# Kernel tuning notes

Measured on AMD Instinct MI355X. Metric: run time of the kernel, lower is better.

## Reference

```python
import jax, jax.numpy as jnp
import numpy as np

B, L, C, H = 2, 4096, 1024, 16
D = C // H
KERNEL_FROM_KN = lambda kn: int(np.sqrt(kn)) + 1


def setup_inputs() -> dict:
    key = jax.random.key(0)
    ks = jax.random.split(key, 4)
    s = 0.02
    kk = KERNEL_FROM_KN(144)  # 13
    return {
        "x": jax.random.normal(ks[0], (B, L, C), jnp.float32),
        "w_qkv": jax.random.normal(ks[1], (C, 3 * C), jnp.float32) * s,
        "b_qkv": jnp.zeros((3 * C,), jnp.float32),
        "rpb": jax.random.normal(ks[2], (H, 2 * kk - 1), jnp.float32) * s,
        "w_proj": jax.random.normal(ks[3], (C, C), jnp.float32) * s,
        "b_proj": jnp.zeros((C,), jnp.float32),
        "k_neighbors": 144,
    }


def reference(x, w_qkv, b_qkv, rpb, w_proj, b_proj, k_neighbors):
    kk = KERNEL_FROM_KN(k_neighbors)  # kernel size (13)
    scale = D ** -0.5
    qkv = (x @ w_qkv + b_qkv).reshape(B, L, 3, H, D).transpose(2, 0, 3, 1, 4)  # (3,B,H,L,D)
    q, k, v = qkv[0] * scale, qkv[1], qkv[2]
    pos = jnp.arange(L)
    # NATTEN window: centered, clamped so the full kernel fits inside [0, L)
    start = jnp.clip(pos - kk // 2, 0, L - kk)               # (L,)
    idx = start[:, None] + jnp.arange(kk)[None, :]           # (L,kk) key positions
    k_win = k[:, :, idx, :]                                  # (B,H,L,kk,D)
    v_win = v[:, :, idx, :]                                  # (B,H,L,kk,D)
    attn = jnp.einsum('bhld,bhlkd->bhlk', q, k_win)          # (B,H,L,kk)
    # relative-position bias index = key_pos - query_pos + (kk - 1) in [0, 2kk-2]
    bias_idx = idx - pos[:, None] + (kk - 1)                 # (L,kk)
    attn = attn + rpb[:, bias_idx][None]                     # broadcast over batch
    attn = jax.nn.softmax(attn, axis=-1)
    out = jnp.einsum('bhlk,bhlkd->bhld', attn, v_win)        # (B,H,L,D)
    out = out.transpose(0, 2, 1, 3).reshape(B, L, C)
    return out @ w_proj + b_proj
```

## Files before the change

### kernel.cpp

```cpp
#include <hip/hip_runtime.h>
#include <hip/hip_bf16.h>
#include <stdint.h>

typedef __bf16 bf16x8 __attribute__((ext_vector_type(8)));
typedef float floatx4 __attribute__((ext_vector_type(4)));

#define B_ 2
#define L_ 4096
#define C_ 1024
#define H_ 16
#define D_ 64
constexpr size_t TEN = (size_t)B_ * H_ * L_ * D_;

__device__ __forceinline__ float bf2f(unsigned short u) {
  union { unsigned int i; float f; } x; x.i = ((unsigned int)u) << 16; return x.f;
}
__device__ __forceinline__ unsigned short f2bf(float f) {
  union { float f; unsigned int i; } x; x.f = f;
  unsigned int i = x.i;
  return (unsigned short)((i + 0x7FFFu + ((i >> 16) & 1u)) >> 16);
}

__device__ __forceinline__ void async_copy16(const unsigned short* g, unsigned short* l) {
  __builtin_amdgcn_global_load_lds(
      (const __attribute__((address_space(1))) unsigned int*)g,
      (__attribute__((address_space(3))) unsigned int*)l,
      16, 0, 0);
}

__global__ __launch_bounds__(256) void cvt_f32_bf16_kernel(
    const float* __restrict__ in, unsigned short* __restrict__ out, int n) {
  int i = (blockIdx.x * 256 + threadIdx.x) * 8;
  if (i >= n) return;
  float4 a = *(const float4*)&in[i];
  float4 b = *(const float4*)&in[i + 4];
  union { uint4 u; unsigned short s[8]; } st;
  st.s[0] = f2bf(a.x); st.s[1] = f2bf(a.y); st.s[2] = f2bf(a.z); st.s[3] = f2bf(a.w);
  st.s[4] = f2bf(b.x); st.s[5] = f2bf(b.y); st.s[6] = f2bf(b.z); st.s[7] = f2bf(b.w);
  *(uint4*)&out[i] = st.u;
}

__global__ __launch_bounds__(256) void transpose_f32_bf16(
    const float* __restrict__ in, unsigned short* __restrict__ out,
    int R, int Ccols) {
  __shared__ float tile[64][65];
  const int bx = blockIdx.x * 64;
  const int by = blockIdx.y * 64;
  const int t = threadIdx.x;
  for (int i = t; i < 1024; i += 256) {
    int r = i >> 4, c4 = (i & 15) << 2;
    float4 v = *(const float4*)&in[(size_t)(by + r) * Ccols + bx + c4];
    tile[r][c4] = v.x; tile[r][c4 + 1] = v.y; tile[r][c4 + 2] = v.z; tile[r][c4 + 3] = v.w;
  }
  __syncthreads();
  for (int i = t; i < 512; i += 256) {
    int r = i >> 3, c8 = (i & 7) << 3;
    union { uint4 u; unsigned short s[8]; } st;
    #pragma unroll
    for (int j = 0; j < 8; ++j) st.s[j] = f2bf(tile[c8 + j][r]);
    *(uint4*)&out[(size_t)(bx + r) * R + by + c8] = st.u;
  }
}

template <int MODE>
__global__ __launch_bounds__(512, 2) void gemm256_kernel(
    const unsigned short* __restrict__ A, const unsigned short* __restrict__ Bt,
    const float* __restrict__ bias, unsigned short* __restrict__ out_bf,
    float* __restrict__ out_f, int M, int N, int K, float qscale) {
  constexpr int BK = 64;
  __shared__ unsigned short ash0[256 * BK], ash1[256 * BK], ash2[256 * BK];
  __shared__ unsigned short bsh0[128 * BK], bsh1[128 * BK], bsh2[128 * BK];

  const int t = threadIdx.x;
  const int nwgx = gridDim.x;
  const int nwg = nwgx * gridDim.y;
  const int flat = blockIdx.y * nwgx + blockIdx.x;
  const int cpx = nwg >> 3;
  const int swz = (flat & 7) * cpx + (flat >> 3);
  const int n0 = (swz % nwgx) * 128;
  const int m0 = (swz / nwgx) * 256;

  const int wave = t >> 6, lane = t & 63;
  const int wr = wave >> 1;
  const int wc = wave & 1;
  const int lm = lane & 15, quad = lane >> 4;

  floatx4 acc[4][4];
  #pragma unroll
  for (int i = 0; i < 4; ++i)
    #pragma unroll
    for (int j = 0; j < 4; ++j) acc[i][j] = (floatx4)0.0f;

#define STAGE(KT, SA, SB) do { \
    _Pragma("unroll") \
    for (int q = 0; q < 4; ++q) { \
      int off = (q * 512 + t) * 8; \
      int r_ = off >> 6; \
      int c_ = (off & 63) ^ ((r_ & 7) << 3); \
      async_copy16(&A[(size_t)(m0 + r_) * K + (KT) + c_], &SA[off]); \
    } \
    _Pragma("unroll") \
    for (int q = 0; q < 2; ++q) { \
      int off = (q * 512 + t) * 8; \
      int r_ = off >> 6; \
      int c_ = (off & 63) ^ ((r_ & 7) << 3); \
      async_copy16(&Bt[(size_t)(n0 + r_) * K + (KT) + c_], &SB[off]); \
    } \
  } while (0)

#define PHASE(ASH, BSH, NH, TAILSTMT) do { \
    bf16x8 af[4][2], bfr[2][2]; \
    _Pragma("unroll") \
    for (int i = 0; i < 4; ++i) { \
      int ra = wr * 64 + i * 16 + lm; \
      _Pragma("unroll") \
      for (int k = 0; k < 2; ++k) \
        af[i][k] = *(const bf16x8*)&ASH[ra * 64 + ((k * 32 + quad * 8) ^ ((ra & 7) << 3))]; \
    } \
    _Pragma("unroll") \
    for (int j = 0; j < 2; ++j) { \
      int rb = wc * 64 + (NH) * 32 + j * 16 + lm; \
      _Pragma("unroll") \
      for (int k = 0; k < 2; ++k) \
        bfr[j][k] = *(const bf16x8*)&BSH[rb * 64 + ((k * 32 + quad * 8) ^ ((rb & 7) << 3))]; \
    } \
    asm volatile("" ::: "memory"); \
    __builtin_amdgcn_s_barrier(); \
    __builtin_amdgcn_s_setprio(1); \
    _Pragma("unroll") \
    for (int k = 0; k < 2; ++k) \
      _Pragma("unroll") \
      for (int i = 0; i < 4; ++i) \
        _Pragma("unroll") \
        for (int j = 0; j < 2; ++j) \
          acc[i][(NH) * 2 + j] = \
              __builtin_amdgcn_mfma_f32_16x16x32_bf16(af[i][k], bfr[j][k], acc[i][(NH) * 2 + j], 0, 0, 0); \
    __builtin_amdgcn_s_setprio(0); \
    TAILSTMT \
    asm volatile("" ::: "memory"); \
    __builtin_amdgcn_s_barrier(); \
  } while (0)

#define WAIT6 asm volatile("s_waitcnt vmcnt(6)" ::: "memory");
#define WAIT0 asm volatile("s_waitcnt vmcnt(0)" ::: "memory");

#define TILE(KT2, ASH, BSH, SAN, SBN, DO_STAGE, TAILSTMT) do { \
    if (DO_STAGE) STAGE((KT2), SAN, SBN); \
    PHASE(ASH, BSH, 0, ;); \
    PHASE(ASH, BSH, 1, TAILSTMT); \
  } while (0)

  STAGE(0, ash0, bsh0);
  STAGE(BK, ash1, bsh1);
  WAIT6
  asm volatile("" ::: "memory");
  __builtin_amdgcn_s_barrier();

  for (int g = 0; g < 4; ++g) {
    int kb = g * 3 * BK;
    TILE(kb + 2 * BK, ash0, bsh0, ash2, bsh2, true, WAIT6);
    TILE(kb + 3 * BK, ash1, bsh1, ash0, bsh0, true, WAIT6);
    TILE(kb + 4 * BK, ash2, bsh2, ash1, bsh1, true, WAIT6);
  }
  TILE(14 * BK, ash0, bsh0, ash2, bsh2, true, WAIT6);
  TILE(15 * BK, ash1, bsh1, ash0, bsh0, true, WAIT6);
  TILE(0,       ash2, bsh2, ash0, bsh0, false, WAIT0);
  TILE(0,       ash0, bsh0, ash1, bsh1, false, ;);

#undef TILE
#undef WAIT0
#undef WAIT6
#undef PHASE
#undef STAGE

  #pragma unroll
  for (int jj = 0; jj < 4; ++jj) {
    int col = n0 + wc * 64 + jj * 16 + lm;
    float bv = bias[col];
    if (MODE == 0) {
      int which = col >> 10;
      int rem = col & 1023;
      int h = rem >> 6, d = rem & 63;
      float mul = (which == 0) ? qscale : 1.0f;
      #pragma unroll
      for (int i = 0; i < 4; ++i)
        #pragma unroll
        for (int r = 0; r < 4; ++r) {
          int row = m0 + wr * 64 + i * 16 + quad * 4 + r;
          int b = row >> 12, l = row & (L_ - 1);
          float v = (acc[i][jj][r] + bv) * mul;
          out_bf[(size_t)which * TEN + (((size_t)(b * H_ + h) * L_ + l) * D_ + d)] = f2bf(v);
        }
    } else {
      #pragma unroll
      for (int i = 0; i < 4; ++i)
        #pragma unroll
        for (int r = 0; r < 4; ++r) {
          int row = m0 + wr * 64 + i * 16 + quad * 4 + r;
          out_f[(size_t)row * N + col] = acc[i][jj][r] + bv;
        }
    }
  }
}

constexpr int KKMAX = 63;
constexpr int TL = 128;
constexpr int LDK = 72;

__global__ __launch_bounds__(256) void natt_kernel(
    const unsigned short* __restrict__ qkv,
    const float* __restrict__ rpb,
    const int* __restrict__ knp,
    unsigned short* __restrict__ attn_out) {
  __shared__ unsigned short k_sh[(TL + KKMAX) * LDK];
  __shared__ unsigned short v_sh[(TL + KKMAX) * LDK];
  __shared__ float rpb_sh[2 * KKMAX + 1];

  const int bh = blockIdx.x;
  const int h = bh & (H_ - 1);
  const int b = bh >> 4;
  const int l0 = blockIdx.y * TL;
  const int t = threadIdx.x;

  int kn = knp[0];
  if (kn > 65536 || kn < 0) {
    union { int i; float f; } u; u.i = kn; kn = (int)u.f;
  }
  int rr = 1;
  while ((rr + 1) * (rr + 1) <= kn) ++rr;
  int kk = rr + 1;
  if (kk > KKMAX) kk = KKMAX;

  int base = l0 - kk / 2;
  if (base < 0) base = 0;
  if (base > L_ - kk) base = L_ - kk;
  int nrows = TL + kk;
  if (nrows > L_ - base) nrows = L_ - base;

  const unsigned short* kg = qkv + TEN + (size_t)bh * L_ * D_;
  const unsigned short* vg = qkv + 2 * TEN + (size_t)bh * L_ * D_;

  for (int i = t; i < nrows * 8; i += 256) {
    int row = i >> 3, c8 = (i & 7) << 3;
    uint4 kv = *(const uint4*)&kg[(size_t)(base + row) * D_ + c8];
    *(uint4*)&k_sh[row * LDK + c8] = kv;
    uint4 vv = *(const uint4*)&vg[(size_t)(base + row) * D_ + c8];
    *(uint4*)&v_sh[row * LDK + c8] = vv;
  }
  int nb = 2 * kk - 1;
  for (int i = t; i < nb; i += 256) rpb_sh[i] = rpb[h * nb + i];
  __syncthreads();

  const int qi = t >> 1, half = t & 1;
  const int l = l0 + qi;

  const unsigned short* qg = qkv + (size_t)bh * L_ * D_ + (size_t)l * D_ + half * 32;
  float qv[32];
  #pragma unroll
  for (int c = 0; c < 4; ++c) {
    union { uint4 u; unsigned short s[8]; } ld;
    ld.u = *(const uint4*)&qg[c * 8];
    #pragma unroll
    for (int j = 0; j < 8; ++j) qv[c * 8 + j] = bf2f(ld.s[j]);
  }

  int start = l - kk / 2;
  if (start < 0) start = 0;
  if (start > L_ - kk) start = L_ - kk;
  const int srow = start - base;
  const int boff = start - l + kk - 1;

  float m = -1e30f, lsum = 0.0f;
  float accv[32];
  #pragma unroll
  for (int d = 0; d < 32; ++d) accv[d] = 0.0f;

  for (int j = 0; j < kk; ++j) {
    const unsigned short* kr = &k_sh[(srow + j) * LDK + half * 32];
    float partial = 0.0f;
    #pragma unroll
    for (int c = 0; c < 4; ++c) {
      union { uint4 u; unsigned short s[8]; } ld;
      ld.u = *(const uint4*)&kr[c * 8];
      #pragma unroll
      for (int jj = 0; jj < 8; ++jj) partial += qv[c * 8 + jj] * bf2f(ld.s[jj]);
    }
    float s = partial + __shfl_xor(partial, 1) + rpb_sh[boff + j];
    float p;
    if (s > m) {
      float corr = __expf(m - s);
      lsum *= corr;
      #pragma unroll
      for (int d = 0; d < 32; ++d) accv[d] *= corr;
      m = s;
      p = 1.0f;
    } else {
      p = __expf(s - m);
    }
    lsum += p;
    const unsigned short* vr = &v_sh[(srow + j) * LDK + half * 32];
    #pragma unroll
    for (int c = 0; c < 4; ++c) {
      union { uint4 u; unsigned short s[8]; } ld;
      ld.u = *(const uint4*)&vr[c * 8];
      #pragma unroll
      for (int jj = 0; jj < 8; ++jj) accv[c * 8 + jj] += p * bf2f(ld.s[jj]);
    }
  }
  float inv = 1.0f / lsum;
  unsigned short* og = attn_out + ((size_t)(b * L_ + l) * C_ + h * D_ + half * 32);
  #pragma unroll
  for (int c = 0; c < 4; ++c) {
    union { uint4 u; unsigned short s[8]; } st;
    #pragma unroll
    for (int jj = 0; jj < 8; ++jj) st.s[jj] = f2bf(accv[c * 8 + jj] * inv);
    *(uint4*)&og[c * 8] = st.u;
  }
}

extern "C" void kernel_launch(void* const* d_in, const int* in_sizes, int n_in,
                              void* d_out, int out_size, void* d_ws, size_t ws_size,
                              hipStream_t stream) {
  const float* x      = (const float*)d_in[0];
  const float* w_qkv  = (const float*)d_in[1];
  const float* b_qkv  = (const float*)d_in[2];
  const float* rpb    = (const float*)d_in[3];
  const float* w_proj = (const float*)d_in[4];
  const float* b_proj = (const float*)d_in[5];
  const int* kn       = (const int*)d_in[6];
  float* out          = (float*)d_out;

  unsigned short* ws      = (unsigned short*)d_ws;
  unsigned short* wT_qkv  = ws;
  unsigned short* wT_proj = wT_qkv + (size_t)3072 * 1024;
  unsigned short* x_bf    = wT_proj + (size_t)1024 * 1024;
  unsigned short* qkv_ws  = x_bf + (size_t)8192 * 1024;
  unsigned short* attn_ws = qkv_ws + 3 * TEN;

  cvt_f32_bf16_kernel<<<(8192 * 1024) / (256 * 8), 256, 0, stream>>>(x, x_bf, 8192 * 1024);
  transpose_f32_bf16<<<dim3(3072 / 64, 1024 / 64), 256, 0, stream>>>(w_qkv, wT_qkv, 1024, 3072);
  transpose_f32_bf16<<<dim3(1024 / 64, 1024 / 64), 256, 0, stream>>>(w_proj, wT_proj, 1024, 1024);
  gemm256_kernel<0><<<dim3(3072 / 128, 8192 / 256), 512, 0, stream>>>(
      x_bf, wT_qkv, b_qkv, qkv_ws, nullptr, 8192, 3072, 1024, 0.125f);
  natt_kernel<<<dim3(B_ * H_, L_ / TL), 256, 0, stream>>>(qkv_ws, rpb, kn, attn_ws);
  gemm256_kernel<1><<<dim3(1024 / 128, 8192 / 256), 512, 0, stream>>>(
      attn_ws, wT_proj, b_proj, nullptr, out, 8192, 1024, 1024, 1.0f);
}
```

Measured before the change: 228.5 us.

## Switch GEMMs to 256x256 tiles with double-buffered eight-phase ping-pong schedule

Both GEMMs now use a 256x256 output tile per workgroup instead of 256x128. Each wave computes a 128x64 sub-tile. The triple-buffered 64-deep K pipeline becomes a double-buffered one, with quarter-tile loads interleaved between four MFMA phases per K step. The aim is more operand reuse per LDS byte and less global traffic per FLOP. The cost is half as many workgroups (fewer for the 1024-wide projection GEMM), more accumulator registers, and a more fragile barrier and waitcnt schedule.

```diff
diff --git a/kernel.cpp b/kernel.cpp
--- a/kernel.cpp
+++ b/kernel.cpp
@@ -63,13 +63,12 @@
 }
 
 template <int MODE>
-__global__ __launch_bounds__(512, 2) void gemm256_kernel(
+__global__ __launch_bounds__(512, 2) void gemm8p_kernel(
     const unsigned short* __restrict__ A, const unsigned short* __restrict__ Bt,
     const float* __restrict__ bias, unsigned short* __restrict__ out_bf,
     float* __restrict__ out_f, int M, int N, int K, float qscale) {
-  constexpr int BK = 64;
-  __shared__ unsigned short ash0[256 * BK], ash1[256 * BK], ash2[256 * BK];
-  __shared__ unsigned short bsh0[128 * BK], bsh1[128 * BK], bsh2[128 * BK];
+  __shared__ unsigned short ash0[256 * 64], bsh0[256 * 64];
+  __shared__ unsigned short ash1[256 * 64], bsh1[256 * 64];
 
   const int t = threadIdx.x;
   const int nwgx = gridDim.x;
@@ -77,105 +76,130 @@
   const int flat = blockIdx.y * nwgx + blockIdx.x;
   const int cpx = nwg >> 3;
   const int swz = (flat & 7) * cpx + (flat >> 3);
-  const int n0 = (swz % nwgx) * 128;
+  const int n0 = (swz % nwgx) * 256;
   const int m0 = (swz / nwgx) * 256;
 
   const int wave = t >> 6, lane = t & 63;
-  const int wr = wave >> 1;
-  const int wc = wave & 1;
+  const int wm = wave >> 2;
+  const int wn = wave & 3;
   const int lm = lane & 15, quad = lane >> 4;
 
-  floatx4 acc[4][4];
-  #pragma unroll
-  for (int i = 0; i < 4; ++i)
+  const int r0 = t >> 3;
+  const int coff = (t & 7) * 8;
+
+  bf16x8 aF[4][2], bF0[2][2], bF1[2][2];
+  floatx4 acc[8][4];
+  #pragma unroll
+  for (int i = 0; i < 8; ++i)
     #pragma unroll
     for (int j = 0; j < 4; ++j) acc[i][j] = (floatx4)0.0f;
 
-#define STAGE(KT, SA, SB) do { \
-    _Pragma("unroll") \
-    for (int q = 0; q < 4; ++q) { \
-      int off = (q * 512 + t) * 8; \
-      int r_ = off >> 6; \
-      int c_ = (off & 63) ^ ((r_ & 7) << 3); \
-      async_copy16(&A[(size_t)(m0 + r_) * K + (KT) + c_], &SA[off]); \
+#define STG_A(QM, KT, DST) do { \
+    _Pragma("unroll") \
+    for (int u = 0; u < 2; ++u) { \
+      int rl = u * 64 + r0; \
+      int c = coff ^ ((rl & 7) << 3); \
+      int gr = m0 + ((rl >> 6) << 7) + (QM) * 64 + (rl & 63); \
+      async_copy16(&A[(size_t)gr * K + (KT) + c], &DST[((QM) * 128 + rl) * 64 + coff]); \
     } \
-    _Pragma("unroll") \
-    for (int q = 0; q < 2; ++q) { \
-      int off = (q * 512 + t) * 8; \
-      int r_ = off >> 6; \
-      int c_ = (off & 63) ^ ((r_ & 7) << 3); \
-      async_copy16(&Bt[(size_t)(n0 + r_) * K + (KT) + c_], &SB[off]); \
+  } while (0)
+#define STG_B(QN, KT, DST) do { \
+    _Pragma("unroll") \
+    for (int u = 0; u < 2; ++u) { \
+      int rl = u * 64 + r0; \
+      int c = coff ^ ((rl & 7) << 3); \
+      int gr = n0 + ((rl >> 5) << 6) + (QN) * 32 + (rl & 31); \
+      async_copy16(&Bt[(size_t)gr * K + (KT) + c], &DST[((QN) * 128 + rl) * 64 + coff]); \
     } \
   } while (0)
 
-#define PHASE(ASH, BSH, NH, TAILSTMT) do { \
-    bf16x8 af[4][2], bfr[2][2]; \
+#define RD_A(QM, SRC) do { \
     _Pragma("unroll") \
     for (int i = 0; i < 4; ++i) { \
-      int ra = wr * 64 + i * 16 + lm; \
+      int rr = (QM) * 128 + wm * 64 + i * 16 + lm; \
       _Pragma("unroll") \
-      for (int k = 0; k < 2; ++k) \
-        af[i][k] = *(const bf16x8*)&ASH[ra * 64 + ((k * 32 + quad * 8) ^ ((ra & 7) << 3))]; \
+      for (int ks = 0; ks < 2; ++ks) \
+        aF[i][ks] = *(const bf16x8*)&SRC[rr * 64 + ((ks * 32 + quad * 8) ^ ((lm & 7) << 3))]; \
     } \
+  } while (0)
+#define RD_B(QN, SRC, BF) do { \
     _Pragma("unroll") \
     for (int j = 0; j < 2; ++j) { \
-      int rb = wc * 64 + (NH) * 32 + j * 16 + lm; \
+      int rr = (QN) * 128 + wn * 32 + j * 16 + lm; \
       _Pragma("unroll") \
-      for (int k = 0; k < 2; ++k) \
-        bfr[j][k] = *(const bf16x8*)&BSH[rb * 64 + ((k * 32 + quad * 8) ^ ((rb & 7) << 3))]; \
+      for (int ks = 0; ks < 2; ++ks) \
+        BF[j][ks] = *(const bf16x8*)&SRC[rr * 64 + ((ks * 32 + quad * 8) ^ ((lm & 7) << 3))]; \
     } \
-    asm volatile("" ::: "memory"); \
-    __builtin_amdgcn_s_barrier(); \
+  } while (0)
+
+#define MMA(IOFF, JOFF, BF) do { \
     __builtin_amdgcn_s_setprio(1); \
     _Pragma("unroll") \
-    for (int k = 0; k < 2; ++k) \
+    for (int ks = 0; ks < 2; ++ks) \
       _Pragma("unroll") \
       for (int i = 0; i < 4; ++i) \
         _Pragma("unroll") \
         for (int j = 0; j < 2; ++j) \
-          acc[i][(NH) * 2 + j] = \
-              __builtin_amdgcn_mfma_f32_16x16x32_bf16(af[i][k], bfr[j][k], acc[i][(NH) * 2 + j], 0, 0, 0); \
+          acc[(IOFF) + i][(JOFF) + j] = __builtin_amdgcn_mfma_f32_16x16x32_bf16( \
+              aF[i][ks], BF[j][ks], acc[(IOFF) + i][(JOFF) + j], 0, 0, 0); \
     __builtin_amdgcn_s_setprio(0); \
-    TAILSTMT \
-    asm volatile("" ::: "memory"); \
-    __builtin_amdgcn_s_barrier(); \
-  } while (0)
-
-#define WAIT6 asm volatile("s_waitcnt vmcnt(6)" ::: "memory");
-#define WAIT0 asm volatile("s_waitcnt vmcnt(0)" ::: "memory");
-
-#define TILE(KT2, ASH, BSH, SAN, SBN, DO_STAGE, TAILSTMT) do { \
-    if (DO_STAGE) STAGE((KT2), SAN, SBN); \
-    PHASE(ASH, BSH, 0, ;); \
-    PHASE(ASH, BSH, 1, TAILSTMT); \
-  } while (0)
-
-  STAGE(0, ash0, bsh0);
-  STAGE(BK, ash1, bsh1);
-  WAIT6
-  asm volatile("" ::: "memory");
-  __builtin_amdgcn_s_barrier();
-
-  for (int g = 0; g < 4; ++g) {
-    int kb = g * 3 * BK;
-    TILE(kb + 2 * BK, ash0, bsh0, ash2, bsh2, true, WAIT6);
-    TILE(kb + 3 * BK, ash1, bsh1, ash0, bsh0, true, WAIT6);
-    TILE(kb + 4 * BK, ash2, bsh2, ash1, bsh1, true, WAIT6);
-  }
-  TILE(14 * BK, ash0, bsh0, ash2, bsh2, true, WAIT6);
-  TILE(15 * BK, ash1, bsh1, ash0, bsh0, true, WAIT6);
-  TILE(0,       ash2, bsh2, ash0, bsh0, false, WAIT0);
-  TILE(0,       ash0, bsh0, ash1, bsh1, false, ;);
-
-#undef TILE
-#undef WAIT0
-#undef WAIT6
-#undef PHASE
-#undef STAGE
+  } while (0)
+
+#define FEN asm volatile("" ::: "memory")
+#define BAR do { FEN; __builtin_amdgcn_s_barrier(); FEN; } while (0)
+#define LGKM0 asm volatile("s_waitcnt lgkmcnt(0)" ::: "memory")
+#define VMC(NN) asm volatile("s_waitcnt vmcnt(" #NN ")" ::: "memory")
+
+#define TILE_STEADY(CURA, CURB, NXTA, KT1, KT2) do { \
+    STG_A(1, (KT1), NXTA); RD_A(0, CURA); RD_B(0, CURB, bF0); \
+    BAR; LGKM0; MMA(0, 0, bF0); BAR; \
+    STG_A(0, (KT2), CURA); RD_B(1, CURB, bF1); \
+    BAR; LGKM0; MMA(0, 2, bF1); BAR; \
+    STG_B(0, (KT2), CURB); RD_A(1, CURA); \
+    BAR; LGKM0; MMA(4, 2, bF1); BAR; \
+    STG_B(1, (KT2), CURB); VMC(6); \
+    BAR; MMA(4, 0, bF0); BAR; \
+  } while (0)
+
+  STG_A(0, 0, ash0); STG_B(0, 0, bsh0); STG_B(1, 0, bsh0); STG_A(1, 0, ash0);
+  STG_A(0, 64, ash1); STG_B(0, 64, bsh1); STG_B(1, 64, bsh1);
+  VMC(6); BAR;
+
+  for (int g = 0; g < 7; ++g) {
+    int kt1 = (2 * g + 1) * 64, kt2 = (2 * g + 2) * 64;
+    TILE_STEADY(ash0, bsh0, ash1, kt1, kt2);
+    TILE_STEADY(ash1, bsh1, ash0, kt1 + 64, kt2 + 64);
+  }
+  STG_A(1, 15 * 64, ash1); RD_A(0, ash0); RD_B(0, bsh0, bF0);
+  BAR; LGKM0; MMA(0, 0, bF0); BAR;
+  RD_B(1, bsh0, bF1);
+  BAR; LGKM0; MMA(0, 2, bF1); BAR;
+  RD_A(1, ash0);
+  BAR; LGKM0; MMA(4, 2, bF1); BAR;
+  VMC(0);
+  BAR; MMA(4, 0, bF0); BAR;
+  RD_A(0, ash1); RD_B(0, bsh1, bF0);
+  BAR; LGKM0; MMA(0, 0, bF0); BAR;
+  RD_B(1, bsh1, bF1);
+  BAR; LGKM0; MMA(0, 2, bF1); BAR;
+  RD_A(1, ash1);
+  BAR; LGKM0; MMA(4, 2, bF1); BAR;
+  MMA(4, 0, bF0);
+
+#undef TILE_STEADY
+#undef VMC
+#undef LGKM0
+#undef BAR
+#undef FEN
+#undef MMA
+#undef RD_B
+#undef RD_A
+#undef STG_B
+#undef STG_A
 
   #pragma unroll
   for (int jj = 0; jj < 4; ++jj) {
-    int col = n0 + wc * 64 + jj * 16 + lm;
+    int col = n0 + wn * 64 + jj * 16 + lm;
     float bv = bias[col];
     if (MODE == 0) {
       int which = col >> 10;
@@ -183,20 +207,20 @@
       int h = rem >> 6, d = rem & 63;
       float mul = (which == 0) ? qscale : 1.0f;
       #pragma unroll
-      for (int i = 0; i < 4; ++i)
+      for (int i = 0; i < 8; ++i)
         #pragma unroll
         for (int r = 0; r < 4; ++r) {
-          int row = m0 + wr * 64 + i * 16 + quad * 4 + r;
+          int row = m0 + wm * 128 + i * 16 + quad * 4 + r;
           int b = row >> 12, l = row & (L_ - 1);
           float v = (acc[i][jj][r] + bv) * mul;
           out_bf[(size_t)which * TEN + (((size_t)(b * H_ + h) * L_ + l) * D_ + d)] = f2bf(v);
         }
     } else {
       #pragma unroll
-      for (int i = 0; i < 4; ++i)
+      for (int i = 0; i < 8; ++i)
         #pragma unroll
         for (int r = 0; r < 4; ++r) {
-          int row = m0 + wr * 64 + i * 16 + quad * 4 + r;
+          int row = m0 + wm * 128 + i * 16 + quad * 4 + r;
           out_f[(size_t)row * N + col] = acc[i][jj][r] + bv;
         }
     }
@@ -340,9 +364,9 @@
   cvt_f32_bf16_kernel<<<(8192 * 1024) / (256 * 8), 256, 0, stream>>>(x, x_bf, 8192 * 1024);
   transpose_f32_bf16<<<dim3(3072 / 64, 1024 / 64), 256, 0, stream>>>(w_qkv, wT_qkv, 1024, 3072);
   transpose_f32_bf16<<<dim3(1024 / 64, 1024 / 64), 256, 0, stream>>>(w_proj, wT_proj, 1024, 1024);
-  gemm256_kernel<0><<<dim3(3072 / 128, 8192 / 256), 512, 0, stream>>>(
+  gemm8p_kernel<0><<<dim3(3072 / 256, 8192 / 256), 512, 0, stream>>>(
       x_bf, wT_qkv, b_qkv, qkv_ws, nullptr, 8192, 3072, 1024, 0.125f);
   natt_kernel<<<dim3(B_ * H_, L_ / TL), 256, 0, stream>>>(qkv_ws, rpb, kn, attn_ws);
-  gemm256_kernel<1><<<dim3(1024 / 128, 8192 / 256), 512, 0, stream>>>(
+  gemm8p_kernel<1><<<dim3(1024 / 256, 8192 / 256), 512, 0, stream>>>(
       attn_ws, wT_proj, b_proj, nullptr, out, 8192, 1024, 1024, 1.0f);
 }
```

Result: slower. 242.7 us (+6.2%).
